# Performance work log

Hardware: AMD Instinct MI355X
Metric: run time of the kernel (lower is better)

## Reference

```python
import jax, jax.numpy as jnp
import numpy as np

B, L, D = 8, 2048, 1024


def setup_inputs() -> dict:
    key = jax.random.key(0)
    kq, kk, kv, km, kw1, kb1, kw2, kb2 = jax.random.split(key, 8)
    q = jax.random.normal(kq, (B, L, D), dtype=jnp.float32)
    k = jax.random.normal(kk, (B, L, D), dtype=jnp.float32)
    v = jax.random.normal(kv, (B, L, D), dtype=jnp.float32)
    attn_mask = jax.random.randint(km, (B, L, L), 0, 2).astype(bool)
    # nn.Linear(d_model, 1) params (Kaiming-uniform-ish scale)
    bound = 1.0 / np.sqrt(D)
    W1 = jax.random.uniform(kw1, (D, 1), minval=-bound, maxval=bound, dtype=jnp.float32)
    b1 = jax.random.uniform(kb1, (1,), minval=-bound, maxval=bound, dtype=jnp.float32)
    W2 = jax.random.uniform(kw2, (D, 1), minval=-bound, maxval=bound, dtype=jnp.float32)
    b2 = jax.random.uniform(kb2, (1,), minval=-bound, maxval=bound, dtype=jnp.float32)
    return {"q": q, "k": k, "v": v, "attn_mask": attn_mask,
            "W1": W1, "b1": b1, "W2": W2, "b2": b2}


def reference(q, k, v, attn_mask, W1, b1, W2, b2):
    # linear-to-scalar projections (dropout is identity in eval mode)
    q_s = (q @ W1 + b1)[..., 0]          # [B, L]
    k_s = (k @ W2 + b2)[..., 0]          # [B, L]
    # additive (concat) attention scores via broadcast add -> [B, L, L]
    attn = q_s[:, :, None] + k_s[:, None, :]
    attn = jnp.where(attn_mask, -jnp.inf, attn)
    attn = jax.nn.softmax(attn, axis=-1)
    attn = jnp.where(attn_mask, jnp.float32(0.0), attn)
    out = jnp.einsum('bls,bsd->bld', attn, v)  # bmm(attn, v)
    return out, attn
```

## Files before the change

kernel.cpp:

```cpp
#include <hip/hip_runtime.h>
#include <hip/hip_bf16.h>

#define B 8
#define L 2048
#define D 1024

typedef __bf16 bf16x8 __attribute__((ext_vector_type(8)));
typedef __bf16 bf16x4 __attribute__((ext_vector_type(4)));
typedef float f32x4 __attribute__((ext_vector_type(4)));

typedef __attribute__((address_space(3))) char lds_char;
typedef const __attribute__((address_space(1))) char glob_char;

__global__ __launch_bounds__(256) void proj_kernel(const float* __restrict__ k,
                                                   const float* __restrict__ W2,
                                                   const float* __restrict__ b2,
                                                   float* __restrict__ e) {
    int t = threadIdx.x;
    int wave = t >> 6, lane = t & 63;
    int row = blockIdx.x * 4 + wave;
    const float4* k4 = (const float4*)(k + (size_t)row * D);
    const float4* w4 = (const float4*)W2;
    float p = 0.f;
#pragma unroll
    for (int s = 0; s < 4; s++) {
        float4 a = k4[s * 64 + lane];
        float4 w = w4[s * 64 + lane];
        p += a.x * w.x + a.y * w.y + a.z * w.z + a.w * w.w;
    }
    for (int off = 32; off > 0; off >>= 1)
        p += __shfl_down(p, off, 64);
    if (lane == 0) e[row] = __expf(p + b2[0]);
}

__global__ __launch_bounds__(256) void transpose_v(const float* __restrict__ v,
                                                   __bf16* __restrict__ vT) {
    __shared__ float tile[32][33];
    int b = blockIdx.z;
    int j0 = blockIdx.y * 32;
    int d0 = blockIdx.x * 32;
    int t = threadIdx.x;
    int jl = t >> 3;
    int dl = (t & 7) * 4;
    float4 val = *(const float4*)(v + ((size_t)b * L + j0 + jl) * D + d0 + dl);
    tile[jl][dl + 0] = val.x;
    tile[jl][dl + 1] = val.y;
    tile[jl][dl + 2] = val.z;
    tile[jl][dl + 3] = val.w;
    __syncthreads();
    int dl2 = t >> 3;
    int jl2 = (t & 7) * 4;
    bf16x4 o;
    o[0] = (__bf16)tile[jl2 + 0][dl2];
    o[1] = (__bf16)tile[jl2 + 1][dl2];
    o[2] = (__bf16)tile[jl2 + 2][dl2];
    o[3] = (__bf16)tile[jl2 + 3][dl2];
    *(bf16x4*)(vT + ((size_t)b * D + d0 + dl2) * L + j0 + jl2) = o;
}

__global__ __launch_bounds__(256) void row_kernel(const int* __restrict__ mask,
                                                  const float* __restrict__ e,
                                                  float* __restrict__ attn,
                                                  __bf16* __restrict__ P) {
    __shared__ float red[4];
    __shared__ float zsh;
    int bid = blockIdx.x;
    int b = bid >> 11;
    int t = threadIdx.x;
    const int4* m4 = (const int4*)(mask + (size_t)bid * L);
    const float4* e4 = (const float4*)(e + (size_t)b * L);
    float4 wv[2];
    float z = 0.f;
#pragma unroll
    for (int s = 0; s < 2; s++) {
        int idx = s * 256 + t;
        int4 mm = m4[idx];
        float4 ee = e4[idx];
        float4 ww;
        ww.x = mm.x ? 0.f : ee.x;
        ww.y = mm.y ? 0.f : ee.y;
        ww.z = mm.z ? 0.f : ee.z;
        ww.w = mm.w ? 0.f : ee.w;
        wv[s] = ww;
        z += ww.x + ww.y + ww.z + ww.w;
    }
    for (int off = 32; off > 0; off >>= 1)
        z += __shfl_down(z, off, 64);
    int wid = t >> 6, lane = t & 63;
    if (lane == 0) red[wid] = z;
    __syncthreads();
    if (t == 0) zsh = 1.f / (red[0] + red[1] + red[2] + red[3]);
    __syncthreads();
    float invZ = zsh;
    float4* a4 = (float4*)(attn + (size_t)bid * L);
    __bf16* prow = P + (size_t)bid * L;
#pragma unroll
    for (int s = 0; s < 2; s++) {
        int idx = s * 256 + t;
        float4 aa;
        aa.x = wv[s].x * invZ;
        aa.y = wv[s].y * invZ;
        aa.z = wv[s].z * invZ;
        aa.w = wv[s].w * invZ;
        a4[idx] = aa;
        bf16x4 pp;
        pp[0] = (__bf16)aa.x;
        pp[1] = (__bf16)aa.y;
        pp[2] = (__bf16)aa.z;
        pp[3] = (__bf16)aa.w;
        *(bf16x4*)(prow + idx * 4) = pp;
    }
}

#define BM 256
#define BN 128
#define BK 64

__global__ __launch_bounds__(256, 2) void gemm_kernel(const __bf16* __restrict__ P,
                                                      const __bf16* __restrict__ vT,
                                                      float* __restrict__ out) {
    __shared__ __bf16 As[BM][BK];
    __shared__ __bf16 Bs[BN][BK];

    int p = blockIdx.x;
    int b = p & 7;
    int q = p >> 3;
    int i0 = (q & 7) * BM;
    int d0 = (q >> 3) * BN;

    int t = threadIdx.x;
    int wave = t >> 6, lane = t & 63;
    const __bf16* Ab = P + ((size_t)b * L + i0) * L;
    const __bf16* Bb = vT + ((size_t)b * D + d0) * L;

    f32x4 acc[4][8];
#pragma unroll
    for (int ti = 0; ti < 4; ti++)
#pragma unroll
        for (int tj = 0; tj < 8; tj++)
            acc[ti][tj] = (f32x4){0.f, 0.f, 0.f, 0.f};

    int lrow = lane & 15;
    int kq = lane >> 4;
    int sx = lrow & 7;

    for (int k0 = 0; k0 < L; k0 += BK) {
        __syncthreads();
#pragma unroll
        for (int s = 0; s < 8; s++) {
            int cbase = s * 256 + wave * 64;
            int c = cbase + lane;
            int r = c >> 3;
            int off = ((c ^ r) & 7) * 8;
            const __bf16* ga = Ab + (size_t)r * L + k0 + off;
            __builtin_amdgcn_global_load_lds((glob_char*)ga,
                                             (lds_char*)((char*)As + cbase * 16),
                                             16, 0, 0);
        }
#pragma unroll
        for (int s = 0; s < 4; s++) {
            int cbase = s * 256 + wave * 64;
            int c = cbase + lane;
            int r = c >> 3;
            int off = ((c ^ r) & 7) * 8;
            const __bf16* gb = Bb + (size_t)r * L + k0 + off;
            __builtin_amdgcn_global_load_lds((glob_char*)gb,
                                             (lds_char*)((char*)Bs + cbase * 16),
                                             16, 0, 0);
        }
        __syncthreads();

#pragma unroll
        for (int kk = 0; kk < 2; kk++) {
            bf16x8 af[4];
#pragma unroll
            for (int ti = 0; ti < 4; ti++) {
                int rowA = wave * 64 + ti * 16 + lrow;
                af[ti] = *(const bf16x8*)((const char*)As + rowA * 128 +
                                          ((((kk << 2) | kq) ^ sx) * 16));
            }
#pragma unroll
            for (int tj = 0; tj < 8; tj++) {
                int rowB = tj * 16 + lrow;
                bf16x8 bfr = *(const bf16x8*)((const char*)Bs + rowB * 128 +
                                              ((((kk << 2) | kq) ^ sx) * 16));
#pragma unroll
                for (int ti = 0; ti < 4; ti++)
                    acc[ti][tj] = __builtin_amdgcn_mfma_f32_16x16x32_bf16(
                        af[ti], bfr, acc[ti][tj], 0, 0, 0);
            }
        }
    }

    int col = lane & 15;
    int rquad = (lane >> 4) * 4;
#pragma unroll
    for (int ti = 0; ti < 4; ti++) {
#pragma unroll
        for (int tj = 0; tj < 8; tj++) {
#pragma unroll
            for (int r = 0; r < 4; r++) {
                int row = i0 + wave * 64 + ti * 16 + rquad + r;
                int c2 = d0 + tj * 16 + col;
                out[((size_t)b * L + row) * D + c2] = acc[ti][tj][r];
            }
        }
    }
}

extern "C" void kernel_launch(void* const* d_in, const int* in_sizes, int n_in,
                              void* d_out, int out_size, void* d_ws, size_t ws_size,
                              hipStream_t stream) {
    const float* k = (const float*)d_in[1];
    const float* v = (const float*)d_in[2];
    const int* mask = (const int*)d_in[3];
    const float* W2 = (const float*)d_in[6];
    const float* b2 = (const float*)d_in[7];

    float* out = (float*)d_out;
    float* attn = out + (size_t)B * L * D;

    char* wp = (char*)d_ws;
    float* e = (float*)wp;             wp += (size_t)B * L * 4;
    __bf16* vT = (__bf16*)wp;          wp += (size_t)B * D * L * 2;
    __bf16* P = (__bf16*)wp;           wp += (size_t)B * L * L * 2;

    proj_kernel<<<B * L / 4, 256, 0, stream>>>(k, W2, b2, e);
    transpose_v<<<dim3(D / 32, L / 32, B), 256, 0, stream>>>(v, vT);
    row_kernel<<<B * L, 256, 0, stream>>>(mask, e, attn, P);
    gemm_kernel<<<512, 256, 0, stream>>>(P, vT, out);
}
```

Measured before the change: 489.5 us.

## Enlarge GEMM tile to 256x256 with 4-slot multi-stage LDS pipeline

The P·V GEMM now uses 512-thread blocks computing 256x256 output tiles with BK=32. It keeps a 4-slot LDS ring buffer, prefetching two stages ahead through global_load_lds. Explicit vmcnt waits plus a single barrier per iteration replace the previous load-then-sync-then-compute loop, so global loads overlap MFMA work. It also raises wave priority around the MFMA block and uses a new XOR swizzle for the 64-byte rows. The cost is 128KB of LDS per block, which limits occupancy to one block per CU, and a grid of only 256 blocks.

```diff
diff --git a/kernel.cpp b/kernel.cpp
--- a/kernel.cpp
+++ b/kernel.cpp
@@ -113,14 +113,15 @@
 }
 
 #define BM 256
-#define BN 128
-#define BK 64
-
-__global__ __launch_bounds__(256, 2) void gemm_kernel(const __bf16* __restrict__ P,
+#define BN 256
+#define BK 32
+#define NT (L / BK)
+
+__global__ __launch_bounds__(512, 2) void gemm_kernel(const __bf16* __restrict__ P,
                                                       const __bf16* __restrict__ vT,
                                                       float* __restrict__ out) {
-    __shared__ __bf16 As[BM][BK];
-    __shared__ __bf16 Bs[BN][BK];
+    __shared__ __bf16 As[4][BM][BK];
+    __shared__ __bf16 Bs[4][BN][BK];
 
     int p = blockIdx.x;
     int b = p & 7;
@@ -130,78 +131,92 @@
 
     int t = threadIdx.x;
     int wave = t >> 6, lane = t & 63;
+    int wm = wave >> 2;
+    int wn = wave & 3;
     const __bf16* Ab = P + ((size_t)b * L + i0) * L;
     const __bf16* Bb = vT + ((size_t)b * D + d0) * L;
 
-    f32x4 acc[4][8];
-#pragma unroll
-    for (int ti = 0; ti < 4; ti++)
-#pragma unroll
-        for (int tj = 0; tj < 8; tj++)
+    f32x4 acc[8][4];
+#pragma unroll
+    for (int ti = 0; ti < 8; ti++)
+#pragma unroll
+        for (int tj = 0; tj < 4; tj++)
             acc[ti][tj] = (f32x4){0.f, 0.f, 0.f, 0.f};
 
     int lrow = lane & 15;
     int kq = lane >> 4;
-    int sx = lrow & 7;
-
-    for (int k0 = 0; k0 < L; k0 += BK) {
-        __syncthreads();
-#pragma unroll
-        for (int s = 0; s < 8; s++) {
-            int cbase = s * 256 + wave * 64;
-            int c = cbase + lane;
-            int r = c >> 3;
-            int off = ((c ^ r) & 7) * 8;
-            const __bf16* ga = Ab + (size_t)r * L + k0 + off;
-            __builtin_amdgcn_global_load_lds((glob_char*)ga,
-                                             (lds_char*)((char*)As + cbase * 16),
-                                             16, 0, 0);
-        }
-#pragma unroll
-        for (int s = 0; s < 4; s++) {
-            int cbase = s * 256 + wave * 64;
-            int c = cbase + lane;
-            int r = c >> 3;
-            int off = ((c ^ r) & 7) * 8;
-            const __bf16* gb = Bb + (size_t)r * L + k0 + off;
-            __builtin_amdgcn_global_load_lds((glob_char*)gb,
-                                             (lds_char*)((char*)Bs + cbase * 16),
-                                             16, 0, 0);
-        }
-        __syncthreads();
-
-#pragma unroll
-        for (int kk = 0; kk < 2; kk++) {
-            bf16x8 af[4];
-#pragma unroll
-            for (int ti = 0; ti < 4; ti++) {
-                int rowA = wave * 64 + ti * 16 + lrow;
-                af[ti] = *(const bf16x8*)((const char*)As + rowA * 128 +
-                                          ((((kk << 2) | kq) ^ sx) * 16));
-            }
-#pragma unroll
-            for (int tj = 0; tj < 8; tj++) {
-                int rowB = tj * 16 + lrow;
-                bf16x8 bfr = *(const bf16x8*)((const char*)Bs + rowB * 128 +
-                                              ((((kk << 2) | kq) ^ sx) * 16));
-#pragma unroll
-                for (int ti = 0; ti < 4; ti++)
-                    acc[ti][tj] = __builtin_amdgcn_mfma_f32_16x16x32_bf16(
-                        af[ti], bfr, acc[ti][tj], 0, 0, 0);
-            }
-        }
-    }
+
+#define STAGE(tt) do {                                                         \
+        int k0_ = (tt) * BK; int sl_ = (tt) & 3;                               \
+        _Pragma("unroll")                                                      \
+        for (int s_ = 0; s_ < 2; s_++) {                                       \
+            int cbase_ = s_ * 512 + wave * 64;                                 \
+            int c_ = cbase_ + lane;                                            \
+            int r_ = c_ >> 2;                                                  \
+            int off_ = ((c_ ^ (r_ >> 1)) & 3) * 8;                             \
+            __builtin_amdgcn_global_load_lds(                                  \
+                (glob_char*)(Ab + (size_t)r_ * L + k0_ + off_),                \
+                (lds_char*)((char*)&As[sl_][0][0] + cbase_ * 16), 16, 0, 0);   \
+            __builtin_amdgcn_global_load_lds(                                  \
+                (glob_char*)(Bb + (size_t)r_ * L + k0_ + off_),                \
+                (lds_char*)((char*)&Bs[sl_][0][0] + cbase_ * 16), 16, 0, 0);   \
+        }                                                                      \
+    } while (0)
+
+#define COMPUTE(tt) do {                                                       \
+        int sl_ = (tt) & 3;                                                    \
+        bf16x8 af[8];                                                          \
+        _Pragma("unroll")                                                      \
+        for (int ti = 0; ti < 8; ti++) {                                       \
+            int rowA_ = wm * 128 + ti * 16 + lrow;                             \
+            af[ti] = *(const bf16x8*)((const char*)&As[sl_][0][0] +            \
+                      rowA_ * 64 + (((kq ^ (rowA_ >> 1)) & 3) << 4));          \
+        }                                                                      \
+        __builtin_amdgcn_s_setprio(1);                                         \
+        _Pragma("unroll")                                                      \
+        for (int tj = 0; tj < 4; tj++) {                                       \
+            int rowB_ = wn * 64 + tj * 16 + lrow;                              \
+            bf16x8 bfr = *(const bf16x8*)((const char*)&Bs[sl_][0][0] +        \
+                          rowB_ * 64 + (((kq ^ (rowB_ >> 1)) & 3) << 4));      \
+            _Pragma("unroll")                                                  \
+            for (int ti = 0; ti < 8; ti++)                                     \
+                acc[ti][tj] = __builtin_amdgcn_mfma_f32_16x16x32_bf16(         \
+                    af[ti], bfr, acc[ti][tj], 0, 0, 0);                        \
+        }                                                                      \
+        __builtin_amdgcn_s_setprio(0);                                         \
+    } while (0)
+
+    STAGE(0);
+    STAGE(1);
+    for (int tt = 0; tt < NT - 2; tt++) {
+        STAGE(tt + 2);
+        asm volatile("s_waitcnt vmcnt(8)" ::: "memory");
+        __builtin_amdgcn_s_barrier();
+        __builtin_amdgcn_sched_barrier(0);
+        COMPUTE(tt);
+    }
+    asm volatile("s_waitcnt vmcnt(4)" ::: "memory");
+    __builtin_amdgcn_s_barrier();
+    __builtin_amdgcn_sched_barrier(0);
+    COMPUTE(NT - 2);
+    asm volatile("s_waitcnt vmcnt(0)" ::: "memory");
+    __builtin_amdgcn_s_barrier();
+    __builtin_amdgcn_sched_barrier(0);
+    COMPUTE(NT - 1);
+
+#undef STAGE
+#undef COMPUTE
 
     int col = lane & 15;
     int rquad = (lane >> 4) * 4;
 #pragma unroll
-    for (int ti = 0; ti < 4; ti++) {
-#pragma unroll
-        for (int tj = 0; tj < 8; tj++) {
+    for (int ti = 0; ti < 8; ti++) {
+#pragma unroll
+        for (int tj = 0; tj < 4; tj++) {
 #pragma unroll
             for (int r = 0; r < 4; r++) {
-                int row = i0 + wave * 64 + ti * 16 + rquad + r;
-                int c2 = d0 + tj * 16 + col;
+                int row = i0 + wm * 128 + ti * 16 + rquad + r;
+                int c2 = d0 + wn * 64 + tj * 16 + col;
                 out[((size_t)b * L + row) * D + c2] = acc[ti][tj][r];
             }
         }
@@ -228,5 +243,5 @@
     proj_kernel<<<B * L / 4, 256, 0, stream>>>(k, W2, b2, e);
     transpose_v<<<dim3(D / 32, L / 32, B), 256, 0, stream>>>(v, vT);
     row_kernel<<<B * L, 256, 0, stream>>>(mask, e, attn, P);
-    gemm_kernel<<<512, 256, 0, stream>>>(P, vT, out);
-}
+    gemm_kernel<<<256, 512, 0, stream>>>(P, vT, out);
+}
```

New measurement: 494.9 us. About the same (+1.1%).
